# Kernel optimization log

Hardware: AMD Instinct MI355X
Metric: run time of the kernel (lower is better)

The kernel has to match this reference:

```python
import jax, jax.numpy as jnp
import numpy as np

B, T, C = 4, 2048, 1024
N_HEADS = 16
HEAD_DIM = C // N_HEADS

def setup_inputs() -> dict:
    key = jax.random.key(0)
    k1, k2, k3 = jax.random.split(key, 3)
    x = jax.random.normal(k1, (B, T, C), dtype=jnp.float32)
    w_attn = jax.random.normal(k2, (C, 3 * C), dtype=jnp.float32) * (1.0 / np.sqrt(C))
    b_attn = jnp.zeros((3 * C,), dtype=jnp.float32)
    w_proj = jax.random.normal(k3, (C, C), dtype=jnp.float32) * (1.0 / np.sqrt(C))
    b_proj = jnp.zeros((C,), dtype=jnp.float32)
    return {"x": x, "w_attn": w_attn, "b_attn": b_attn, "w_proj": w_proj, "b_proj": b_proj}

def reference(x, w_attn, b_attn, w_proj, b_proj):
    Bx, Tx, Cx = x.shape
    qkv = x @ w_attn + b_attn                      # [B,T,3C]
    q, k, v = jnp.split(qkv, 3, axis=-1)
    def heads(t):
        return t.reshape(Bx, Tx, N_HEADS, HEAD_DIM).transpose(0, 2, 1, 3)  # [B,H,T,D]
    q, k, v = heads(q), heads(k), heads(v)
    scale = 1.0 / np.sqrt(HEAD_DIM)
    attn = jnp.einsum('bhqd,bhkd->bhqk', q, k) * scale  # [B,H,T,T]
    causal = jnp.tril(jnp.ones((Tx, Tx), dtype=bool))
    attn = jnp.where(causal[None, None, :, :], attn, -jnp.inf)
    attn = jax.nn.softmax(attn, axis=-1)
    out = jnp.einsum('bhqk,bhkd->bhqd', attn, v)        # [B,H,T,D]
    out = out.transpose(0, 2, 1, 3).reshape(Bx, Tx, Cx)
    return out @ w_proj + b_proj
```

## Files before the change

### kernel.cpp

```cpp
#include <hip/hip_runtime.h>
#include <hip/hip_bf16.h>

#define BATCH 4
#define SEQ   2048
#define CH    1024
#define NH    16
#define HD    64
#define BT    8192

typedef __attribute__((ext_vector_type(8))) short bf16x8;
typedef __attribute__((ext_vector_type(4))) float f32x4;
typedef __attribute__((ext_vector_type(16))) float f32x16;

__device__ __forceinline__ unsigned short f2b(float f) {
  __hip_bfloat16 h = __float2bfloat16(f);
  return *reinterpret_cast<unsigned short*>(&h);
}

__device__ __forceinline__ unsigned cvt_pk(float lo, float hi_) {
  unsigned r;
  asm("v_cvt_pk_bf16_f32 %0, %1, %2" : "=v"(r) : "v"(lo), "v"(hi_));
  return r;
}
__device__ __forceinline__ void plane_swap(unsigned &a, unsigned &b) {
  asm("v_permlane32_swap_b32 %0, %1" : "+v"(a), "+v"(b));
}


__global__ void conv_x_bf16(const float* __restrict__ in, unsigned short* __restrict__ out, int n4) {
  int i = blockIdx.x * blockDim.x + threadIdx.x;
  if (i >= n4) return;
  float4 v = reinterpret_cast<const float4*>(in)[i];
  ushort4 o;
  o.x = f2b(v.x); o.y = f2b(v.y); o.z = f2b(v.z); o.w = f2b(v.w);
  reinterpret_cast<ushort4*>(out)[i] = o;
}

__global__ void transpose_w_bf16(const float* __restrict__ in, unsigned short* __restrict__ out,
                                 int R, int Cc) {
  __shared__ float tile[32][33];
  int c0 = blockIdx.x * 32, r0 = blockIdx.y * 32;
  int tx = threadIdx.x, ty = threadIdx.y;
  #pragma unroll
  for (int i = 0; i < 32; i += 8)
    tile[ty + i][tx] = in[(size_t)(r0 + ty + i) * Cc + c0 + tx];
  __syncthreads();
  #pragma unroll
  for (int i = 0; i < 32; i += 8)
    out[(size_t)(c0 + ty + i) * R + r0 + tx] = f2b(tile[tx][ty + i]);
}


#define QSCALE 0.18033688011112042f

#define GSTAGE64(BUF, K0)                                                                      \
  {                                                                                            \
    _Pragma("unroll")                                                                          \
    for (int c = 0; c < 4; ++c) {                                                              \
      int idx = c * 256 + tid;                                                                 \
      int row = idx >> 3;                                                                      \
      int cg = (idx & 7) ^ (row & 7);                                                          \
      const unsigned short* sA = A + (size_t)(m0 + row) * 1024 + (K0) + cg * 8;                \
      __builtin_amdgcn_global_load_lds((const __attribute__((address_space(1))) void*)sA,      \
          (__attribute__((address_space(3))) void*)&sb[(BUF) * 8192 + (c * 256 + (tid & ~63)) * 8], 16, 0, 0); \
      const unsigned short* sB = Bt + (size_t)(n0 + row) * 1024 + (K0) + cg * 8;               \
      __builtin_amdgcn_global_load_lds((const __attribute__((address_space(1))) void*)sB,      \
          (__attribute__((address_space(3))) void*)&sb[16384 + (BUF) * 8192 + (c * 256 + (tid & ~63)) * 8], 16, 0, 0); \
    }                                                                                          \
  }

#define GEMM_MAIN_LOOP                                                                         \
  GSTAGE64(0, 0)                                                                               \
  asm volatile("s_waitcnt vmcnt(0)" ::: "memory");                                             \
  __builtin_amdgcn_s_barrier();                                                                \
  int cur = 0;                                                                                 \
  for (int k0 = 0; k0 < 1024; k0 += 64) {                                                      \
    if (k0 + 64 < 1024) GSTAGE64(cur ^ 1, k0 + 64)                                             \
    _Pragma("unroll")                                                                          \
    for (int sub = 0; sub < 2; ++sub) {                                                        \
      bf16x8 a[4], b[4];                                                                       \
      _Pragma("unroll")                                                                        \
      for (int i = 0; i < 4; ++i) {                                                            \
        int row = wr * 64 + i * 16 + lr;                                                       \
        a[i] = *reinterpret_cast<const bf16x8*>(                                               \
            &sb[cur * 8192 + row * 64 + (((sub * 4 + lh) ^ (lr & 7)) << 3)]);                  \
      }                                                                                        \
      _Pragma("unroll")                                                                        \
      for (int j = 0; j < 4; ++j) {                                                            \
        int row = wc * 64 + j * 16 + lr;                                                       \
        b[j] = *reinterpret_cast<const bf16x8*>(                                               \
            &sb[16384 + cur * 8192 + row * 64 + (((sub * 4 + lh) ^ (lr & 7)) << 3)]);          \
      }                                                                                        \
      _Pragma("unroll")                                                                        \
      for (int i = 0; i < 4; ++i)                                                              \
        _Pragma("unroll")                                                                      \
        for (int j = 0; j < 4; ++j)                                                            \
          acc[i][j] = __builtin_amdgcn_mfma_f32_16x16x32_bf16(a[i], b[j], acc[i][j], 0, 0, 0); \
    }                                                                                          \
    asm volatile("s_waitcnt vmcnt(0)" ::: "memory");                                           \
    __builtin_amdgcn_s_barrier();                                                              \
    cur ^= 1;                                                                                  \
  }

__global__ __launch_bounds__(256) void gemm_qkv(
    const unsigned short* __restrict__ A,
    const unsigned short* __restrict__ Bt,
    const float* __restrict__ bias,
    unsigned short* __restrict__ Qb,
    unsigned short* __restrict__ Kb,
    unsigned short* __restrict__ Vt) {
  __shared__ __align__(16) unsigned short sb[32768];
  int tid = threadIdx.x;
  int lane = tid & 63, wav = tid >> 6;
  int wr = wav >> 1, wc = wav & 1;
  int lr = lane & 15, lh = lane >> 4;
  int m0 = blockIdx.x * 128, n0 = blockIdx.y * 128;

  f32x4 acc[4][4];
  #pragma unroll
  for (int i = 0; i < 4; ++i)
    #pragma unroll
    for (int j = 0; j < 4; ++j)
      acc[i][j] = f32x4{0.f, 0.f, 0.f, 0.f};

  GEMM_MAIN_LOOP

  int which = n0 >> 10;
  int h2 = (n0 >> 6) & 15;
  int bb = m0 >> 11, t0 = m0 & 2047;

  if (which < 2) {
    unsigned short* dst = which ? Kb : Qb;
    float sc = which ? 1.0f : QSCALE;
    size_t headbase = (size_t)(bb * 16 + h2 + wc) * SEQ;
    #pragma unroll
    for (int j = 0; j < 4; ++j) {
      int d = j * 16 + lr;
      float bv = bias[n0 + wc * 64 + d];
      #pragma unroll
      for (int i = 0; i < 4; ++i) {
        #pragma unroll
        for (int r = 0; r < 4; ++r) {
          int t = t0 + wr * 64 + i * 16 + lh * 4 + r;
          dst[(headbase + t) * HD + d] = f2b((acc[i][j][r] + bv) * sc);
        }
      }
    }
  } else {
    unsigned short* tile = sb;
    #pragma unroll
    for (int j = 0; j < 4; ++j) {
      int d = wc * 64 + j * 16 + lr;
      float bv = bias[n0 + d];
      int sw = d & 7;
      #pragma unroll
      for (int i = 0; i < 4; ++i) {
        int cm = wr * 16 + i * 4 + lh;
        unsigned lo = cvt_pk(acc[i][j][0] + bv, acc[i][j][1] + bv);
        unsigned hi_ = cvt_pk(acc[i][j][2] + bv, acc[i][j][3] + bv);
        unsigned long long val = (unsigned long long)lo | ((unsigned long long)hi_ << 32);
        *reinterpret_cast<unsigned long long*>(&tile[d * 128 + ((cm ^ sw) << 2)]) = val;
      }
    }
    __syncthreads();
    #pragma unroll
    for (int it = 0; it < 8; ++it) {
      int pid = it * 256 + tid;
      int drow = pid >> 4, p = pid & 15;
      int sw = drow & 7;
      union { unsigned long long u[2]; bf16x8 v; } u;
      u.u[0] = *reinterpret_cast<const unsigned long long*>(&tile[drow * 128 + (((2 * p) ^ sw) << 2)]);
      u.u[1] = *reinterpret_cast<const unsigned long long*>(&tile[drow * 128 + ((((2 * p) ^ sw) ^ 1) << 2)]);
      *reinterpret_cast<bf16x8*>(
          &Vt[((size_t)(bb * 16 + h2 + (drow >> 6)) * 64 + (drow & 63)) * SEQ + t0 + p * 8]) = u.v;
    }
  }
}


__global__ __launch_bounds__(512, 2) void attn_fwd(
    const unsigned short* __restrict__ Qb,
    const unsigned short* __restrict__ Kb,
    const unsigned short* __restrict__ Vt,
    unsigned short* __restrict__ AO) {
  __shared__ __align__(16) unsigned short sbuf[32768];

  int tid = threadIdx.x;
  int lane = tid & 63, w = tid >> 6;
  int ql = lane & 31, hi = lane >> 5;
  int bid = blockIdx.x;
  int head = bid & 63;
  int qs = 7 - (bid >> 6);
  int q0 = qs * 256;
  int NT = 2 * (qs + 1);
  int b = head >> 4, h = head & 15;

  const unsigned short* Qh = Qb + (size_t)head * SEQ * HD;
  const unsigned short* Kh = Kb + (size_t)head * SEQ * HD;
  const unsigned short* Vh = Vt + (size_t)head * HD * SEQ;

#define STAGE128(BUF, KV0)                                                                     \
  {                                                                                            \
    _Pragma("unroll")                                                                          \
    for (int c = 0; c < 2; ++c) {                                                              \
      int idx = c * 512 + tid;                                                                 \
      int krow = idx >> 3;                                                                     \
      int kcg = (idx & 7) ^ (krow & 7);                                                        \
      const unsigned short* srcK_ = Kh + (size_t)((KV0) + krow) * HD + kcg * 8;                \
      __builtin_amdgcn_global_load_lds((const __attribute__((address_space(1))) void*)srcK_,   \
          (__attribute__((address_space(3))) void*)&sbuf[(BUF) * 8192 + (c * 512 + (tid & ~63)) * 8], 16, 0, 0); \
      int vrow = idx >> 4;                                                                     \
      int vcg = (idx & 15) ^ (vrow & 15);                                                      \
      const unsigned short* srcV_ = Vh + (size_t)vrow * SEQ + (KV0) + vcg * 8;                 \
      __builtin_amdgcn_global_load_lds((const __attribute__((address_space(1))) void*)srcV_,   \
          (__attribute__((address_space(3))) void*)&sbuf[16384 + (BUF) * 8192 + (c * 512 + (tid & ~63)) * 8], 16, 0, 0); \
    }                                                                                          \
  }

  int qg = q0 + w * 32 + ql;
  bf16x8 qf[4];
  #pragma unroll
  for (int dblk = 0; dblk < 4; ++dblk)
    qf[dblk] = *reinterpret_cast<const bf16x8*>(&Qh[(size_t)qg * HD + dblk * 16 + hi * 8]);

  f32x16 o0 = (f32x16)0.0f, o1 = (f32x16)0.0f;
  float lrun = 0.f;

  STAGE128(0, 0)
  asm volatile("s_waitcnt vmcnt(0)" ::: "memory");
  __builtin_amdgcn_s_barrier();

  int cur = 0;
  int wq_hi = q0 + w * 32 + 31;
  for (int t = 0; t < NT; ++t) {
    int tkv0 = t * 128;
    if (t + 1 < NT) STAGE128(cur ^ 1, tkv0 + 128)

    #pragma unroll
    for (int sub = 0; sub < 2; ++sub) {
      int kv0 = tkv0 + sub * 64;
      if (kv0 <= wq_hi) {
        f32x16 s0 = (f32x16)0.0f, s1 = (f32x16)0.0f;
        int rk0 = sub * 64 + ql, rk1 = sub * 64 + 32 + ql;
        __builtin_amdgcn_s_setprio(1);
        #pragma unroll
        for (int dblk = 0; dblk < 4; ++dblk) {
          bf16x8 kf0 = *reinterpret_cast<const bf16x8*>(
              &sbuf[cur * 8192 + rk0 * 64 + (((dblk * 2 + hi) ^ (rk0 & 7)) << 3)]);
          s0 = __builtin_amdgcn_mfma_f32_32x32x16_bf16(kf0, qf[dblk], s0, 0, 0, 0);
          bf16x8 kf1 = *reinterpret_cast<const bf16x8*>(
              &sbuf[cur * 8192 + rk1 * 64 + (((dblk * 2 + hi) ^ (rk1 & 7)) << 3)]);
          s1 = __builtin_amdgcn_mfma_f32_32x32x16_bf16(kf1, qf[dblk], s1, 0, 0, 0);
        }
        __builtin_amdgcn_s_setprio(0);

        float p[32];
        bool needMask = (kv0 + 63 > q0 + 32 * w);
        #pragma unroll
        for (int r = 0; r < 16; ++r) {
          int cr = (r & 3) + 8 * (r >> 2);
          float v0 = s0[r], v1 = s1[r];
          if (needMask) {
            int kv_ = kv0 + 4 * hi + cr;
            v0 = (kv_ > qg) ? -1e30f : v0;
            v1 = (kv_ + 32 > qg) ? -1e30f : v1;
          }
          p[r] = __builtin_amdgcn_exp2f(v0);
          p[16 + r] = __builtin_amdgcn_exp2f(v1);
        }

        float a16[16], a8[8], a4[4];
        #pragma unroll
        for (int i = 0; i < 16; ++i) a16[i] = p[i] + p[i + 16];
        #pragma unroll
        for (int i = 0; i < 8; ++i) a8[i] = a16[i] + a16[i + 8];
        #pragma unroll
        for (int i = 0; i < 4; ++i) a4[i] = a8[i] + a8[i + 4];
        float rs = (a4[0] + a4[1]) + (a4[2] + a4[3]);
        rs += __shfl_xor(rs, 32);
        lrun += rs;

        union FU { unsigned u[4]; bf16x8 v; };
        FU fr[4];
        #pragma unroll
        for (int blk = 0; blk < 2; ++blk) {
          unsigned X = cvt_pk(p[blk * 16 + 0], p[blk * 16 + 1]);
          unsigned Z = cvt_pk(p[blk * 16 + 4], p[blk * 16 + 5]);
          plane_swap(X, Z);
          unsigned Y = cvt_pk(p[blk * 16 + 2], p[blk * 16 + 3]);
          unsigned W = cvt_pk(p[blk * 16 + 6], p[blk * 16 + 7]);
          plane_swap(Y, W);
          fr[blk * 2].u[0] = X; fr[blk * 2].u[1] = Y; fr[blk * 2].u[2] = Z; fr[blk * 2].u[3] = W;
          unsigned X2 = cvt_pk(p[blk * 16 + 8], p[blk * 16 + 9]);
          unsigned Z2 = cvt_pk(p[blk * 16 + 12], p[blk * 16 + 13]);
          plane_swap(X2, Z2);
          unsigned Y2 = cvt_pk(p[blk * 16 + 10], p[blk * 16 + 11]);
          unsigned W2 = cvt_pk(p[blk * 16 + 14], p[blk * 16 + 15]);
          plane_swap(Y2, W2);
          fr[blk * 2 + 1].u[0] = X2; fr[blk * 2 + 1].u[1] = Y2;
          fr[blk * 2 + 1].u[2] = Z2; fr[blk * 2 + 1].u[3] = W2;
        }

        __builtin_amdgcn_s_setprio(1);
        #pragma unroll
        for (int kc = 0; kc < 4; ++kc) {
          int rd0 = ql, rd1 = 32 + ql;
          int gch = sub * 8 + (kc << 1) + hi;
          bf16x8 vf0 = *reinterpret_cast<const bf16x8*>(
              &sbuf[16384 + cur * 8192 + rd0 * 128 + ((gch ^ (rd0 & 15)) << 3)]);
          o0 = __builtin_amdgcn_mfma_f32_32x32x16_bf16(vf0, fr[kc].v, o0, 0, 0, 0);
          bf16x8 vf1 = *reinterpret_cast<const bf16x8*>(
              &sbuf[16384 + cur * 8192 + rd1 * 128 + ((gch ^ (rd1 & 15)) << 3)]);
          o1 = __builtin_amdgcn_mfma_f32_32x32x16_bf16(vf1, fr[kc].v, o1, 0, 0, 0);
        }
        __builtin_amdgcn_s_setprio(0);
      }
    }

    asm volatile("s_waitcnt vmcnt(0)" ::: "memory");
    __builtin_amdgcn_s_barrier();
    cur ^= 1;
  }

  float inv = 1.0f / lrun;
  int qloc = w * 32 + ql;
  #pragma unroll
  for (int dblk = 0; dblk < 2; ++dblk) {
    #pragma unroll
    for (int m = 0; m < 4; ++m) {
      float v0, v1, v2, v3;
      if (dblk == 0) {
        v0 = o0[m * 4 + 0] * inv; v1 = o0[m * 4 + 1] * inv;
        v2 = o0[m * 4 + 2] * inv; v3 = o0[m * 4 + 3] * inv;
      } else {
        v0 = o1[m * 4 + 0] * inv; v1 = o1[m * 4 + 1] * inv;
        v2 = o1[m * 4 + 2] * inv; v3 = o1[m * 4 + 3] * inv;
      }
      unsigned u0 = (unsigned)f2b(v0) | ((unsigned)f2b(v1) << 16);
      unsigned u1 = (unsigned)f2b(v2) | ((unsigned)f2b(v3) << 16);
      int slot = (dblk * 4 + m) ^ (qloc & 7);
      unsigned long long val = (unsigned long long)u0 | ((unsigned long long)u1 << 32);
      *reinterpret_cast<unsigned long long*>(&sbuf[qloc * 64 + slot * 8 + hi * 4]) = val;
    }
  }
  __syncthreads();

  #pragma unroll
  for (int it = 0; it < 4; ++it) {
    int qr = it * 64 + (tid >> 3);
    int lc = tid & 7;
    int slot = lc ^ (qr & 7);
    bf16x8 v = *reinterpret_cast<const bf16x8*>(&sbuf[qr * 64 + slot * 8]);
    *reinterpret_cast<bf16x8*>(
        &AO[(size_t)(b * SEQ + q0 + qr) * CH + h * 64 + lc * 8]) = v;
  }
}


__global__ __launch_bounds__(256) void gemm_proj(
    const unsigned short* __restrict__ A,
    const unsigned short* __restrict__ Bt,
    const float* __restrict__ bias,
    float* __restrict__ out) {
  __shared__ __align__(16) unsigned short sb[32768];
  int tid = threadIdx.x;
  int lane = tid & 63, wav = tid >> 6;
  int wr = wav >> 1, wc = wav & 1;
  int lr = lane & 15, lh = lane >> 4;
  int m0 = blockIdx.x * 128, n0 = blockIdx.y * 128;

  f32x4 acc[4][4];
  #pragma unroll
  for (int i = 0; i < 4; ++i)
    #pragma unroll
    for (int j = 0; j < 4; ++j)
      acc[i][j] = f32x4{0.f, 0.f, 0.f, 0.f};

  GEMM_MAIN_LOOP

  #pragma unroll
  for (int i = 0; i < 4; ++i) {
    #pragma unroll
    for (int j = 0; j < 4; ++j) {
      int n = n0 + wc * 64 + j * 16 + lr;
      float bv = bias[n];
      #pragma unroll
      for (int r = 0; r < 4; ++r) {
        int m = m0 + wr * 64 + i * 16 + lh * 4 + r;
        out[(size_t)m * 1024 + n] = acc[i][j][r] + bv;
      }
    }
  }
}


extern "C" void kernel_launch(void* const* d_in, const int* in_sizes, int n_in,
                              void* d_out, int out_size, void* d_ws, size_t ws_size,
                              hipStream_t stream) {
  const float* x      = (const float*)d_in[0];
  const float* w_attn = (const float*)d_in[1];
  const float* b_attn = (const float*)d_in[2];
  const float* w_proj = (const float*)d_in[3];
  const float* b_proj = (const float*)d_in[4];
  float* out = (float*)d_out;

  char* ws = (char*)d_ws;
  unsigned short* xb  = (unsigned short*)(ws);
  unsigned short* wAT = (unsigned short*)(ws + 16777216);
  unsigned short* wPT = (unsigned short*)(ws + 23068672);
  unsigned short* Qb  = (unsigned short*)(ws + 25165824);
  unsigned short* Kb  = (unsigned short*)(ws + 41943040);
  unsigned short* Vt  = (unsigned short*)(ws + 58720256);
  unsigned short* AO  = (unsigned short*)(ws + 75497472);

  conv_x_bf16<<<(BT * CH / 4 + 255) / 256, 256, 0, stream>>>(x, xb, BT * CH / 4);
  transpose_w_bf16<<<dim3(3 * CH / 32, CH / 32), dim3(32, 8), 0, stream>>>(w_attn, wAT, CH, 3 * CH);
  transpose_w_bf16<<<dim3(CH / 32, CH / 32), dim3(32, 8), 0, stream>>>(w_proj, wPT, CH, CH);
  gemm_qkv<<<dim3(BT / 128, 3 * CH / 128), 256, 0, stream>>>(xb, wAT, b_attn, Qb, Kb, Vt);
  attn_fwd<<<512, 512, 0, stream>>>(Qb, Kb, Vt, AO);
  gemm_proj<<<dim3(BT / 128, CH / 128), 256, 0, stream>>>(AO, wPT, b_proj, out);
}
```

Before: 150.2 us.

## Use 256x128 GEMM tiles with 8 waves and triple-buffered LDS pipeline

```diff
diff --git a/kernel.cpp b/kernel.cpp
--- a/kernel.cpp
+++ b/kernel.cpp
@@ -53,68 +53,102 @@
 
 #define QSCALE 0.18033688011112042f
 
-#define GSTAGE64(BUF, K0)                                                                      \
-  {                                                                                            \
-    _Pragma("unroll")                                                                          \
-    for (int c = 0; c < 4; ++c) {                                                              \
-      int idx = c * 256 + tid;                                                                 \
-      int row = idx >> 3;                                                                      \
-      int cg = (idx & 7) ^ (row & 7);                                                          \
-      const unsigned short* sA = A + (size_t)(m0 + row) * 1024 + (K0) + cg * 8;                \
-      __builtin_amdgcn_global_load_lds((const __attribute__((address_space(1))) void*)sA,      \
-          (__attribute__((address_space(3))) void*)&sb[(BUF) * 8192 + (c * 256 + (tid & ~63)) * 8], 16, 0, 0); \
-      const unsigned short* sB = Bt + (size_t)(n0 + row) * 1024 + (K0) + cg * 8;               \
-      __builtin_amdgcn_global_load_lds((const __attribute__((address_space(1))) void*)sB,      \
-          (__attribute__((address_space(3))) void*)&sb[16384 + (BUF) * 8192 + (c * 256 + (tid & ~63)) * 8], 16, 0, 0); \
-    }                                                                                          \
-  }
-
-#define GEMM_MAIN_LOOP                                                                         \
-  GSTAGE64(0, 0)                                                                               \
-  asm volatile("s_waitcnt vmcnt(0)" ::: "memory");                                             \
+#define GST_A(BUF, K0, L)                                                                      \
+  { int idx_ = (L) * 512 + tid;                                                                \
+    int row_ = idx_ >> 3;                                                                      \
+    int cg_ = (idx_ & 7) ^ (row_ & 7);                                                         \
+    const unsigned short* s_ = A + (size_t)(m0 + row_) * 1024 + (K0) + cg_ * 8;                \
+    __builtin_amdgcn_global_load_lds((const __attribute__((address_space(1))) void*)s_,        \
+        (__attribute__((address_space(3))) void*)&sb[(BUF) * 24576 + ((L) * 512 + (tid & ~63)) * 8], 16, 0, 0); }
+
+#define GST_B(BUF, K0, L)                                                                      \
+  { int idx_ = (L) * 512 + tid;                                                                \
+    int row_ = idx_ >> 3;                                                                      \
+    int cg_ = (idx_ & 7) ^ (row_ & 7);                                                         \
+    const unsigned short* s_ = Bt + (size_t)(n0 + row_) * 1024 + (K0) + cg_ * 8;               \
+    __builtin_amdgcn_global_load_lds((const __attribute__((address_space(1))) void*)s_,        \
+        (__attribute__((address_space(3))) void*)&sb[(BUF) * 24576 + 16384 + ((L) * 512 + (tid & ~63)) * 8], 16, 0, 0); }
+
+#define GST_P1(BUF, K0) GST_A(BUF, K0, 0) GST_A(BUF, K0, 1) GST_A(BUF, K0, 2)
+#define GST_P2(BUF, K0) GST_A(BUF, K0, 3) GST_B(BUF, K0, 0) GST_B(BUF, K0, 1)
+
+#define GEMM256_MAIN                                                                           \
+  GST_P1(0, 0) GST_P2(0, 0)                                                                    \
+  GST_P1(1, 64) GST_P2(1, 64)                                                                  \
+  asm volatile("s_waitcnt vmcnt(6)" ::: "memory");                                             \
   __builtin_amdgcn_s_barrier();                                                                \
   int cur = 0;                                                                                 \
-  for (int k0 = 0; k0 < 1024; k0 += 64) {                                                      \
-    if (k0 + 64 < 1024) GSTAGE64(cur ^ 1, k0 + 64)                                             \
-    _Pragma("unroll")                                                                          \
-    for (int sub = 0; sub < 2; ++sub) {                                                        \
-      bf16x8 a[4], b[4];                                                                       \
+  for (int t = 0; t < 16; ++t) {                                                               \
+    bool st = (t + 2 < 16);                                                                    \
+    int nb = cur + 2; if (nb >= 3) nb -= 3;                                                    \
+    int k2 = t * 64 + 128;                                                                     \
+    bf16x8 bfr[4][2], afr[2][2];                                                               \
+    _Pragma("unroll")                                                                          \
+    for (int j = 0; j < 4; ++j) {                                                              \
+      int row = wc * 64 + j * 16 + lr;                                                         \
       _Pragma("unroll")                                                                        \
-      for (int i = 0; i < 4; ++i) {                                                            \
-        int row = wr * 64 + i * 16 + lr;                                                       \
-        a[i] = *reinterpret_cast<const bf16x8*>(                                               \
-            &sb[cur * 8192 + row * 64 + (((sub * 4 + lh) ^ (lr & 7)) << 3)]);                  \
-      }                                                                                        \
+      for (int sub = 0; sub < 2; ++sub)                                                        \
+        bfr[j][sub] = *reinterpret_cast<const bf16x8*>(                                        \
+            &sb[cur * 24576 + 16384 + row * 64 + (((sub * 4 + lh) ^ (lr & 7)) << 3)]);         \
+    }                                                                                          \
+    _Pragma("unroll")                                                                          \
+    for (int i = 0; i < 2; ++i) {                                                              \
+      int row = wr * 64 + i * 16 + lr;                                                         \
+      _Pragma("unroll")                                                                        \
+      for (int sub = 0; sub < 2; ++sub)                                                        \
+        afr[i][sub] = *reinterpret_cast<const bf16x8*>(                                        \
+            &sb[cur * 24576 + row * 64 + (((sub * 4 + lh) ^ (lr & 7)) << 3)]);                 \
+    }                                                                                          \
+    if (st) { GST_P1(nb, k2) }                                                                 \
+    __builtin_amdgcn_s_barrier();                                                              \
+    __builtin_amdgcn_s_setprio(1);                                                             \
+    _Pragma("unroll")                                                                          \
+    for (int i = 0; i < 2; ++i)                                                                \
       _Pragma("unroll")                                                                        \
       for (int j = 0; j < 4; ++j) {                                                            \
-        int row = wc * 64 + j * 16 + lr;                                                       \
-        b[j] = *reinterpret_cast<const bf16x8*>(                                               \
-            &sb[16384 + cur * 8192 + row * 64 + (((sub * 4 + lh) ^ (lr & 7)) << 3)]);          \
+        acc[i][j] = __builtin_amdgcn_mfma_f32_16x16x32_bf16(afr[i][0], bfr[j][0], acc[i][j], 0, 0, 0); \
+        acc[i][j] = __builtin_amdgcn_mfma_f32_16x16x32_bf16(afr[i][1], bfr[j][1], acc[i][j], 0, 0, 0); \
       }                                                                                        \
+    __builtin_amdgcn_s_setprio(0);                                                             \
+    __builtin_amdgcn_s_barrier();                                                              \
+    _Pragma("unroll")                                                                          \
+    for (int i = 0; i < 2; ++i) {                                                              \
+      int row = wr * 64 + (i + 2) * 16 + lr;                                                   \
       _Pragma("unroll")                                                                        \
-      for (int i = 0; i < 4; ++i)                                                              \
-        _Pragma("unroll")                                                                      \
-        for (int j = 0; j < 4; ++j)                                                            \
-          acc[i][j] = __builtin_amdgcn_mfma_f32_16x16x32_bf16(a[i], b[j], acc[i][j], 0, 0, 0); \
+      for (int sub = 0; sub < 2; ++sub)                                                        \
+        afr[i][sub] = *reinterpret_cast<const bf16x8*>(                                        \
+            &sb[cur * 24576 + row * 64 + (((sub * 4 + lh) ^ (lr & 7)) << 3)]);                 \
     }                                                                                          \
-    asm volatile("s_waitcnt vmcnt(0)" ::: "memory");                                           \
+    if (st) { GST_P2(nb, k2) }                                                                 \
     __builtin_amdgcn_s_barrier();                                                              \
-    cur ^= 1;                                                                                  \
-  }
-
-__global__ __launch_bounds__(256) void gemm_qkv(
+    __builtin_amdgcn_s_setprio(1);                                                             \
+    _Pragma("unroll")                                                                          \
+    for (int i = 0; i < 2; ++i)                                                                \
+      _Pragma("unroll")                                                                        \
+      for (int j = 0; j < 4; ++j) {                                                            \
+        acc[i + 2][j] = __builtin_amdgcn_mfma_f32_16x16x32_bf16(afr[i][0], bfr[j][0], acc[i + 2][j], 0, 0, 0); \
+        acc[i + 2][j] = __builtin_amdgcn_mfma_f32_16x16x32_bf16(afr[i][1], bfr[j][1], acc[i + 2][j], 0, 0, 0); \
+      }                                                                                        \
+    __builtin_amdgcn_s_setprio(0);                                                             \
+    if (st) { asm volatile("s_waitcnt vmcnt(6)" ::: "memory"); }                               \
+    else    { asm volatile("s_waitcnt vmcnt(0)" ::: "memory"); }                               \
+    __builtin_amdgcn_s_barrier();                                                              \
+    cur = (cur + 1 == 3) ? 0 : cur + 1;                                                        \
+  }
+
+__global__ __launch_bounds__(512, 2) void gemm_qkv(
     const unsigned short* __restrict__ A,
     const unsigned short* __restrict__ Bt,
     const float* __restrict__ bias,
     unsigned short* __restrict__ Qb,
     unsigned short* __restrict__ Kb,
     unsigned short* __restrict__ Vt) {
-  __shared__ __align__(16) unsigned short sb[32768];
+  __shared__ __align__(16) unsigned short sb[73728];
   int tid = threadIdx.x;
   int lane = tid & 63, wav = tid >> 6;
   int wr = wav >> 1, wc = wav & 1;
   int lr = lane & 15, lh = lane >> 4;
-  int m0 = blockIdx.x * 128, n0 = blockIdx.y * 128;
+  int m0 = blockIdx.x * 256, n0 = blockIdx.y * 128;
 
   f32x4 acc[4][4];
   #pragma unroll
@@ -123,7 +157,7 @@
     for (int j = 0; j < 4; ++j)
       acc[i][j] = f32x4{0.f, 0.f, 0.f, 0.f};
 
-  GEMM_MAIN_LOOP
+  GEMM256_MAIN
 
   int which = n0 >> 10;
   int h2 = (n0 >> 6) & 15;
@@ -159,18 +193,18 @@
         unsigned lo = cvt_pk(acc[i][j][0] + bv, acc[i][j][1] + bv);
         unsigned hi_ = cvt_pk(acc[i][j][2] + bv, acc[i][j][3] + bv);
         unsigned long long val = (unsigned long long)lo | ((unsigned long long)hi_ << 32);
-        *reinterpret_cast<unsigned long long*>(&tile[d * 128 + ((cm ^ sw) << 2)]) = val;
+        *reinterpret_cast<unsigned long long*>(&tile[d * 256 + ((cm ^ sw) << 2)]) = val;
       }
     }
     __syncthreads();
     #pragma unroll
     for (int it = 0; it < 8; ++it) {
-      int pid = it * 256 + tid;
-      int drow = pid >> 4, p = pid & 15;
+      int pid = it * 512 + tid;
+      int drow = pid >> 5, p = pid & 31;
       int sw = drow & 7;
       union { unsigned long long u[2]; bf16x8 v; } u;
-      u.u[0] = *reinterpret_cast<const unsigned long long*>(&tile[drow * 128 + (((2 * p) ^ sw) << 2)]);
-      u.u[1] = *reinterpret_cast<const unsigned long long*>(&tile[drow * 128 + ((((2 * p) ^ sw) ^ 1) << 2)]);
+      u.u[0] = *reinterpret_cast<const unsigned long long*>(&tile[drow * 256 + (((2 * p) ^ sw) << 2)]);
+      u.u[1] = *reinterpret_cast<const unsigned long long*>(&tile[drow * 256 + ((((2 * p) ^ sw) ^ 1) << 2)]);
       *reinterpret_cast<bf16x8*>(
           &Vt[((size_t)(bb * 16 + h2 + (drow >> 6)) * 64 + (drow & 63)) * SEQ + t0 + p * 8]) = u.v;
     }
@@ -357,17 +391,17 @@
 }
 
 
-__global__ __launch_bounds__(256) void gemm_proj(
+__global__ __launch_bounds__(512, 2) void gemm_proj(
     const unsigned short* __restrict__ A,
     const unsigned short* __restrict__ Bt,
     const float* __restrict__ bias,
     float* __restrict__ out) {
-  __shared__ __align__(16) unsigned short sb[32768];
+  __shared__ __align__(16) unsigned short sb[73728];
   int tid = threadIdx.x;
   int lane = tid & 63, wav = tid >> 6;
   int wr = wav >> 1, wc = wav & 1;
   int lr = lane & 15, lh = lane >> 4;
-  int m0 = blockIdx.x * 128, n0 = blockIdx.y * 128;
+  int m0 = blockIdx.x * 256, n0 = blockIdx.y * 128;
 
   f32x4 acc[4][4];
   #pragma unroll
@@ -376,7 +410,7 @@
     for (int j = 0; j < 4; ++j)
       acc[i][j] = f32x4{0.f, 0.f, 0.f, 0.f};
 
-  GEMM_MAIN_LOOP
+  GEMM256_MAIN
 
   #pragma unroll
   for (int i = 0; i < 4; ++i) {
@@ -416,7 +450,7 @@
   conv_x_bf16<<<(BT * CH / 4 + 255) / 256, 256, 0, stream>>>(x, xb, BT * CH / 4);
   transpose_w_bf16<<<dim3(3 * CH / 32, CH / 32), dim3(32, 8), 0, stream>>>(w_attn, wAT, CH, 3 * CH);
   transpose_w_bf16<<<dim3(CH / 32, CH / 32), dim3(32, 8), 0, stream>>>(w_proj, wPT, CH, CH);
-  gemm_qkv<<<dim3(BT / 128, 3 * CH / 128), 256, 0, stream>>>(xb, wAT, b_attn, Qb, Kb, Vt);
+  gemm_qkv<<<dim3(BT / 256, 3 * CH / 128), 512, 0, stream>>>(xb, wAT, b_attn, Qb, Kb, Vt);
   attn_fwd<<<512, 512, 0, stream>>>(Qb, Kb, Vt, AO);
-  gemm_proj<<<dim3(BT / 128, CH / 128), 256, 0, stream>>>(AO, wPT, b_proj, out);
-}
+  gemm_proj<<<dim3(BT / 256, CH / 128), 512, 0, stream>>>(AO, wPT, b_proj, out);
+}
```

New measurement: 158.1 us. +5.2%, slower.
